# Kernel optimization log

Hardware: AMD Instinct MI355X
Metric: run time of the kernel (lower is better)

## Reference

```python
import jax, jax.numpy as jnp
import numpy as np

B, T, K, C, H = 64, 20, 5, 3, 224  # batch, candidate frames, selected frames, channels, full res
LOWD = T * 3 * 64 * 64             # 245760 flattened low-res clip


def setup_inputs() -> dict:
    key = jax.random.key(0)
    ks = jax.random.split(key, 6)
    return {
        "Full_Frame64": jax.random.normal(ks[0], (B, T, 3, 64, 64), jnp.float32),
        "Full_Frame224": jax.random.normal(ks[1], (B, T, C, H, H), jnp.float32),
        "W_skim": jax.random.normal(ks[2], (LOWD, 64), jnp.float32) * 0.01,
        "b_skim": jnp.zeros((64,), jnp.float32),
        "W_pol": jax.random.normal(ks[3], (64, 20), jnp.float32) * 0.1,
        "b_pol": jnp.zeros((20,), jnp.float32),
        "W_eval": jax.random.normal(ks[4], (K * C, 400), jnp.float32) * 0.1,
        "b_eval": jnp.zeros((400,), jnp.float32),
    }


def reference(Full_Frame64, Full_Frame224, W_skim, b_skim, W_pol, b_pol, W_eval, b_eval):
    # skim_net stub: flatten low-res clip -> 64-d feature
    fea = Full_Frame64.reshape(B, -1) @ W_skim + b_skim                 # [B,64]
    # PolicyNet (per source bug, the inner Linear(64,64) is discarded): relu -> Linear(64,20)
    logits = jax.nn.relu(fea) @ W_pol + b_pol                           # [B,20]
    dist = jax.lax.stop_gradient(jax.nn.softmax(logits, axis=1))        # detached, as in source
    # Test mode: top-5 probabilities, indices sorted ascending
    idx = jnp.sort(jax.lax.top_k(dist, K)[1], axis=1)                   # [B,5] int32
    # gather selected frames: [B,5,3,224,224]
    selected = jnp.take_along_axis(Full_Frame224, idx[:, :, None, None, None], axis=1)
    # eval_net stub: spatial mean pool -> flatten -> Linear(15,400)
    pooled = selected.mean(axis=(3, 4)).reshape(B, K * C)               # [B,15]
    out = pooled @ W_eval + b_eval                                       # [B,400]
    return out
```

## Files before the change

kernel.cpp:

```cpp
#include <hip/hip_runtime.h>
#include <float.h>

#define B_SZ   64
#define T_FR   20
#define K_SEL  5
#define C_CH   3
#define D_SKIM 245760
#define HW224  50176
#define F4_IMG 12544
#define K1_BLOCKS 768
#define K1_TILES  10
#define BK        32
#define GP_PARTS  4
#define F4_PART   3136

#define AC(v, dp) ((dp) == 0 ? (v).x : (dp) == 1 ? (v).y : (dp) == 2 ? (v).z : (v).w)

__global__ __launch_bounds__(256) void skim_gemm(
    const float* __restrict__ A, const float* __restrict__ W,
    float* __restrict__ partial) {
  __shared__ float lds[8192];
  const int t    = threadIdx.x;
  const int lane = t & 63;
  const int wav  = t >> 6;
  const int kb   = lane >> 3;
  const int b0   = kb << 3;
  const int j0   = (lane & 7) << 3;

  const int ga0 = 2 * wav;
  const int arow0 = 8 * ga0 + (lane >> 3);
  const int aslot0 = (lane & 7) ^ (ga0 & 7);
  const int arow1 = 8 * (ga0 + 1) + (lane >> 3);
  const int aslot1 = (lane & 7) ^ ((ga0 + 1) & 7);
  const int wrow0 = 4 * ga0 + (lane >> 4);
  const int wcol0 = (lane & 15) << 2;
  const int wrow1 = 4 * (ga0 + 1) + (lane >> 4);

  float acc[8][8];
#pragma unroll
  for (int i = 0; i < 8; ++i)
#pragma unroll
    for (int j = 0; j < 8; ++j) acc[i][j] = 0.f;

  const long dbase = (long)blockIdx.x * (K1_TILES * BK);

#define STAGE(bufsel, tile_)                                                   \
  {                                                                            \
    const long d0_ = dbase + (long)(tile_) * BK;                               \
    float* Ab = lds + (bufsel) * 4096;                                         \
    float* Wb = Ab + 2048;                                                     \
    __builtin_amdgcn_global_load_lds(                                          \
        (const __attribute__((address_space(1))) void*)(A + (long)arow0 * D_SKIM + d0_ + aslot0 * 4), \
        (__attribute__((address_space(3))) void*)(Ab + ga0 * 256), 16, 0, 0);  \
    __builtin_amdgcn_global_load_lds(                                          \
        (const __attribute__((address_space(1))) void*)(A + (long)arow1 * D_SKIM + d0_ + aslot1 * 4), \
        (__attribute__((address_space(3))) void*)(Ab + (ga0 + 1) * 256), 16, 0, 0); \
    __builtin_amdgcn_global_load_lds(                                          \
        (const __attribute__((address_space(1))) void*)(W + (d0_ + wrow0) * 64 + wcol0), \
        (__attribute__((address_space(3))) void*)(Wb + ga0 * 256), 16, 0, 0);  \
    __builtin_amdgcn_global_load_lds(                                          \
        (const __attribute__((address_space(1))) void*)(W + (d0_ + wrow1) * 64 + wcol0), \
        (__attribute__((address_space(3))) void*)(Wb + (ga0 + 1) * 256), 16, 0, 0); \
  }

  STAGE(0, 0)
  asm volatile("s_waitcnt vmcnt(0)" ::: "memory");
  __syncthreads();

  for (int tile = 0; tile < K1_TILES; ++tile) {
    if (tile + 1 < K1_TILES) STAGE((tile + 1) & 1, tile + 1)
    const float* Ab = lds + (tile & 1) * 4096;
    const float* Wb = Ab + 2048;
#pragma unroll
    for (int chunk = 0; chunk < 2; ++chunk) {
      const int dc = (wav << 3) + (chunk << 2);
      const int sw = dc ^ (kb << 2);
      const float4 a0 = *reinterpret_cast<const float4*>(&Ab[(b0 + 0) * 32 + sw]);
      const float4 a1 = *reinterpret_cast<const float4*>(&Ab[(b0 + 1) * 32 + sw]);
      const float4 a2 = *reinterpret_cast<const float4*>(&Ab[(b0 + 2) * 32 + sw]);
      const float4 a3 = *reinterpret_cast<const float4*>(&Ab[(b0 + 3) * 32 + sw]);
      const float4 a4 = *reinterpret_cast<const float4*>(&Ab[(b0 + 4) * 32 + sw]);
      const float4 a5 = *reinterpret_cast<const float4*>(&Ab[(b0 + 5) * 32 + sw]);
      const float4 a6 = *reinterpret_cast<const float4*>(&Ab[(b0 + 6) * 32 + sw]);
      const float4 a7 = *reinterpret_cast<const float4*>(&Ab[(b0 + 7) * 32 + sw]);
#pragma unroll
      for (int dp = 0; dp < 4; ++dp) {
        const float4 wlo = *reinterpret_cast<const float4*>(&Wb[(dc + dp) * 64 + j0]);
        const float4 whi = *reinterpret_cast<const float4*>(&Wb[(dc + dp) * 64 + j0 + 4]);
#define FMA_ROW(i, av)                             \
        acc[i][0] = fmaf(av, wlo.x, acc[i][0]);    \
        acc[i][1] = fmaf(av, wlo.y, acc[i][1]);    \
        acc[i][2] = fmaf(av, wlo.z, acc[i][2]);    \
        acc[i][3] = fmaf(av, wlo.w, acc[i][3]);    \
        acc[i][4] = fmaf(av, whi.x, acc[i][4]);    \
        acc[i][5] = fmaf(av, whi.y, acc[i][5]);    \
        acc[i][6] = fmaf(av, whi.z, acc[i][6]);    \
        acc[i][7] = fmaf(av, whi.w, acc[i][7]);
        FMA_ROW(0, AC(a0, dp)) FMA_ROW(1, AC(a1, dp))
        FMA_ROW(2, AC(a2, dp)) FMA_ROW(3, AC(a3, dp))
        FMA_ROW(4, AC(a4, dp)) FMA_ROW(5, AC(a5, dp))
        FMA_ROW(6, AC(a6, dp)) FMA_ROW(7, AC(a7, dp))
#undef FMA_ROW
      }
    }
    asm volatile("s_waitcnt vmcnt(0)" ::: "memory");
    __syncthreads();
  }
#undef STAGE

  float* reg = lds + ((wav & 1) ? 4096 : 0);
  if (wav < 2) {
#pragma unroll
    for (int i = 0; i < 8; ++i) {
      *reinterpret_cast<float4*>(&reg[(b0 + i) * 64 + j0])     =
          make_float4(acc[i][0], acc[i][1], acc[i][2], acc[i][3]);
      *reinterpret_cast<float4*>(&reg[(b0 + i) * 64 + j0 + 4]) =
          make_float4(acc[i][4], acc[i][5], acc[i][6], acc[i][7]);
    }
  }
  __syncthreads();
  if (wav >= 2) {
#pragma unroll
    for (int i = 0; i < 8; ++i) {
      float4 lo = *reinterpret_cast<const float4*>(&reg[(b0 + i) * 64 + j0]);
      float4 hi = *reinterpret_cast<const float4*>(&reg[(b0 + i) * 64 + j0 + 4]);
      lo.x += acc[i][0]; lo.y += acc[i][1]; lo.z += acc[i][2]; lo.w += acc[i][3];
      hi.x += acc[i][4]; hi.y += acc[i][5]; hi.z += acc[i][6]; hi.w += acc[i][7];
      *reinterpret_cast<float4*>(&reg[(b0 + i) * 64 + j0])     = lo;
      *reinterpret_cast<float4*>(&reg[(b0 + i) * 64 + j0 + 4]) = hi;
    }
  }
  __syncthreads();
  const float4* r0 = reinterpret_cast<const float4*>(lds);
  const float4* r1 = reinterpret_cast<const float4*>(lds + 4096);
  float4* out = reinterpret_cast<float4*>(partial + (long)blockIdx.x * 4096);
#pragma unroll
  for (int k = 0; k < 4; ++k) {
    const int e = t + k * 256;
    float4 v0 = r0[e], v1 = r1[e];
    out[e] = make_float4(v0.x + v1.x, v0.y + v1.y, v0.z + v1.z, v0.w + v1.w);
  }
}

__global__ __launch_bounds__(256) void policy_topk(
    const float* __restrict__ partial, const float* __restrict__ b_skim,
    const float* __restrict__ W_pol, const float* __restrict__ b_pol,
    int* __restrict__ idx_out) {
  const int b    = blockIdx.x;
  const int t    = threadIdx.x;
  const int lane = t & 63;
  const int wav  = t >> 6;
  __shared__ float red[4][64];
  __shared__ float vsh[64];
  __shared__ float lgsh[20];

  const int P4 = K1_BLOCKS / 4;
  const float* base = partial + (long)(wav * P4) * 4096 + b * 64 + lane;
  float s = 0.f;
#pragma unroll 16
  for (int p = 0; p < P4; ++p) s += base[(long)p * 4096];
  red[wav][lane] = s;
  __syncthreads();

  if (wav == 0) {
    float fea = ((red[0][lane] + red[1][lane]) + (red[2][lane] + red[3][lane]))
                + b_skim[lane];
    vsh[lane] = fmaxf(fea, 0.f);
  }
  __syncthreads();

  if (t < 20) {
    float lg = b_pol[t];
#pragma unroll 8
    for (int k = 0; k < 64; ++k) lg = fmaf(vsh[k], W_pol[k * 20 + t], lg);
    lgsh[t] = lg;
  }
  __syncthreads();

  if (t == 0) {
    float lg[20];
#pragma unroll
    for (int i = 0; i < 20; ++i) lg[i] = lgsh[i];
    int sel[K_SEL];
#pragma unroll
    for (int s5 = 0; s5 < K_SEL; ++s5) {
      int bi = 0; float bv = lg[0];
      for (int i = 1; i < 20; ++i)
        if (lg[i] > bv) { bv = lg[i]; bi = i; }
      sel[s5] = bi; lg[bi] = -FLT_MAX;
    }
#pragma unroll
    for (int a = 1; a < K_SEL; ++a) {
      int v = sel[a], c = a;
      while (c > 0 && sel[c - 1] > v) { sel[c] = sel[c - 1]; --c; }
      sel[c] = v;
    }
#pragma unroll
    for (int s5 = 0; s5 < K_SEL; ++s5) idx_out[b * K_SEL + s5] = sel[s5];
  }
}

__global__ __launch_bounds__(256) void gather_pool(
    const float* __restrict__ F224, const int* __restrict__ idx,
    float* __restrict__ pooled_part) {
  const int blk  = blockIdx.x;
  const int part = blk & 3;
  const int img  = blk >> 2;
  const int b = img / 15;
  const int r = img % 15;
  const int s = r / 3;
  const int c = r % 3;
  const int fr = idx[b * K_SEL + s];
  const float4* p4 = reinterpret_cast<const float4*>(F224) +
      ((long)(b * T_FR + fr) * C_CH + c) * F4_IMG + part * F4_PART;
  float sum = 0.f;
#pragma unroll 4
  for (int i = threadIdx.x; i < F4_PART; i += 256) {
    float4 v = p4[i];
    sum += (v.x + v.y) + (v.z + v.w);
  }
#pragma unroll
  for (int off = 32; off; off >>= 1) sum += __shfl_down(sum, off);
  __shared__ float red[4];
  if ((threadIdx.x & 63) == 0) red[threadIdx.x >> 6] = sum;
  __syncthreads();
  if (threadIdx.x == 0) pooled_part[blk] = (red[0] + red[1]) + (red[2] + red[3]);
}

__global__ __launch_bounds__(512) void eval_gemm(
    const float* __restrict__ pooled_part, const float* __restrict__ W_eval,
    const float* __restrict__ b_eval, float* __restrict__ out) {
  const int b = blockIdx.x;
  const int t = threadIdx.x;
  __shared__ float sh[60];
  __shared__ float pk[15];
  if (t < 60) sh[t] = pooled_part[b * 60 + t];
  __syncthreads();
  if (t < 15)
    pk[t] = ((sh[t * 4] + sh[t * 4 + 1]) + (sh[t * 4 + 2] + sh[t * 4 + 3]))
            * (1.0f / HW224);
  __syncthreads();
  if (t < 400) {
    float o = b_eval[t];
#pragma unroll
    for (int k = 0; k < 15; ++k) o = fmaf(pk[k], W_eval[k * 400 + t], o);
    out[b * 400 + t] = o;
  }
}

extern "C" void kernel_launch(void* const* d_in, const int* in_sizes, int n_in,
                              void* d_out, int out_size, void* d_ws, size_t ws_size,
                              hipStream_t stream) {
  const float* F64    = (const float*)d_in[0];
  const float* F224   = (const float*)d_in[1];
  const float* W_skim = (const float*)d_in[2];
  const float* b_skim = (const float*)d_in[3];
  const float* W_pol  = (const float*)d_in[4];
  const float* b_pol  = (const float*)d_in[5];
  const float* W_eval = (const float*)d_in[6];
  const float* b_eval = (const float*)d_in[7];
  float* out = (float*)d_out;

  char* ws = (char*)d_ws;
  float* partial     = (float*)ws;
  int*   idx         = (int*)(ws + (size_t)K1_BLOCKS * 4096 * 4);
  float* pooled_part = (float*)(ws + (size_t)K1_BLOCKS * 4096 * 4 + 1280);

  skim_gemm  <<<K1_BLOCKS, 256, 0, stream>>>(F64, W_skim, partial);
  policy_topk<<<B_SZ, 256, 0, stream>>>(partial, b_skim, W_pol, b_pol, idx);
  gather_pool<<<B_SZ * K_SEL * C_CH * GP_PARTS, 256, 0, stream>>>(F224, idx, pooled_part);
  eval_gemm  <<<B_SZ, 512, 0, stream>>>(pooled_part, W_eval, b_eval, out);
}
```

Measured before the change: 85.11 us.

## Fuse policy and eval stages via atomic arrival counters, triple-buffer skim GEMM

```diff
diff --git a/kernel.cpp b/kernel.cpp
--- a/kernel.cpp
+++ b/kernel.cpp
@@ -16,10 +16,13 @@
 
 #define AC(v, dp) ((dp) == 0 ? (v).x : (dp) == 1 ? (v).y : (dp) == 2 ? (v).z : (v).w)
 
-__global__ __launch_bounds__(256) void skim_gemm(
+__global__ __launch_bounds__(256) void skim_policy(
     const float* __restrict__ A, const float* __restrict__ W,
-    float* __restrict__ partial) {
-  __shared__ float lds[8192];
+    float* __restrict__ partial, const float* __restrict__ b_skim,
+    const float* __restrict__ W_pol, const float* __restrict__ b_pol,
+    int* __restrict__ idx_out, int* __restrict__ cnt) {
+  __shared__ float lds[12288];
+  __shared__ int s_arr;
   const int t    = threadIdx.x;
   const int lane = t & 63;
   const int wav  = t >> 6;
@@ -27,14 +30,14 @@
   const int b0   = kb << 3;
   const int j0   = (lane & 7) << 3;
 
-  const int ga0 = 2 * wav;
-  const int arow0 = 8 * ga0 + (lane >> 3);
+  const int ga0    = 2 * wav;
+  const int arow0  = 8 * ga0 + (lane >> 3);
   const int aslot0 = (lane & 7) ^ (ga0 & 7);
-  const int arow1 = 8 * (ga0 + 1) + (lane >> 3);
+  const int arow1  = 8 * (ga0 + 1) + (lane >> 3);
   const int aslot1 = (lane & 7) ^ ((ga0 + 1) & 7);
-  const int wrow0 = 4 * ga0 + (lane >> 4);
-  const int wcol0 = (lane & 15) << 2;
-  const int wrow1 = 4 * (ga0 + 1) + (lane >> 4);
+  const int wrow0  = 4 * ga0 + (lane >> 4);
+  const int wcol0  = (lane & 15) << 2;
+  const int wrow1  = 4 * (ga0 + 1) + (lane >> 4);
 
   float acc[8][8];
 #pragma unroll
@@ -64,12 +67,18 @@
   }
 
   STAGE(0, 0)
-  asm volatile("s_waitcnt vmcnt(0)" ::: "memory");
-  __syncthreads();
+  STAGE(1, 1)
 
   for (int tile = 0; tile < K1_TILES; ++tile) {
-    if (tile + 1 < K1_TILES) STAGE((tile + 1) & 1, tile + 1)
-    const float* Ab = lds + (tile & 1) * 4096;
+    if (tile < K1_TILES - 1) {
+      asm volatile("s_waitcnt vmcnt(4)" ::: "memory");
+    } else {
+      asm volatile("s_waitcnt vmcnt(0)" ::: "memory");
+    }
+    __builtin_amdgcn_sched_barrier(0);
+    __builtin_amdgcn_s_barrier();
+    if (tile + 2 < K1_TILES) STAGE((tile + 2) % 3, tile + 2)
+    const float* Ab = lds + (tile % 3) * 4096;
     const float* Wb = Ab + 2048;
 #pragma unroll
     for (int chunk = 0; chunk < 2; ++chunk) {
@@ -103,11 +112,10 @@
 #undef FMA_ROW
       }
     }
-    asm volatile("s_waitcnt vmcnt(0)" ::: "memory");
-    __syncthreads();
   }
 #undef STAGE
 
+  __syncthreads();
   float* reg = lds + ((wav & 1) ? 4096 : 0);
   if (wav < 2) {
 #pragma unroll
@@ -131,39 +139,44 @@
     }
   }
   __syncthreads();
-  const float4* r0 = reinterpret_cast<const float4*>(lds);
-  const float4* r1 = reinterpret_cast<const float4*>(lds + 4096);
-  float4* out = reinterpret_cast<float4*>(partial + (long)blockIdx.x * 4096);
-#pragma unroll
-  for (int k = 0; k < 4; ++k) {
-    const int e = t + k * 256;
-    float4 v0 = r0[e], v1 = r1[e];
-    out[e] = make_float4(v0.x + v1.x, v0.y + v1.y, v0.z + v1.z, v0.w + v1.w);
-  }
-}
-
-__global__ __launch_bounds__(256) void policy_topk(
-    const float* __restrict__ partial, const float* __restrict__ b_skim,
-    const float* __restrict__ W_pol, const float* __restrict__ b_pol,
-    int* __restrict__ idx_out) {
-  const int b    = blockIdx.x;
-  const int t    = threadIdx.x;
-  const int lane = t & 63;
-  const int wav  = t >> 6;
-  __shared__ float red[4][64];
-  __shared__ float vsh[64];
-  __shared__ float lgsh[20];
-
+  {
+    const float4* r0 = reinterpret_cast<const float4*>(lds);
+    const float4* r1 = reinterpret_cast<const float4*>(lds + 4096);
+    float4* outp = reinterpret_cast<float4*>(partial + (long)blockIdx.x * 4096);
+#pragma unroll
+    for (int k = 0; k < 4; ++k) {
+      const int e = t + k * 256;
+      float4 v0 = r0[e], v1 = r1[e];
+      outp[e] = make_float4(v0.x + v1.x, v0.y + v1.y, v0.z + v1.z, v0.w + v1.w);
+    }
+  }
+
+  __syncthreads();
+  if (t == 0)
+    s_arr = __hip_atomic_fetch_add(cnt, 1, __ATOMIC_ACQ_REL, __HIP_MEMORY_SCOPE_AGENT);
+  __syncthreads();
+  const int arr = s_arr;
+  if (arr < K1_BLOCKS - B_SZ) return;
+  const int b = arr - (K1_BLOCKS - B_SZ);
+
+  if (t == 0) {
+    while (__hip_atomic_load(cnt, __ATOMIC_ACQUIRE, __HIP_MEMORY_SCOPE_AGENT) < K1_BLOCKS) {}
+  }
+  __syncthreads();
+
+  float* red  = lds;
+  float* vsh  = lds + 256;
+  float* lgsh = lds + 320;
   const int P4 = K1_BLOCKS / 4;
   const float* base = partial + (long)(wav * P4) * 4096 + b * 64 + lane;
-  float s = 0.f;
+  float ssum = 0.f;
 #pragma unroll 16
-  for (int p = 0; p < P4; ++p) s += base[(long)p * 4096];
-  red[wav][lane] = s;
+  for (int p = 0; p < P4; ++p) ssum += base[(long)p * 4096];
+  red[wav * 64 + lane] = ssum;
   __syncthreads();
 
   if (wav == 0) {
-    float fea = ((red[0][lane] + red[1][lane]) + (red[2][lane] + red[3][lane]))
+    float fea = ((red[lane] + red[64 + lane]) + (red[128 + lane] + red[192 + lane]))
                 + b_skim[lane];
     vsh[lane] = fmaxf(fea, 0.f);
   }
@@ -200,9 +213,11 @@
   }
 }
 
-__global__ __launch_bounds__(256) void gather_pool(
+__global__ __launch_bounds__(256) void gather_eval(
     const float* __restrict__ F224, const int* __restrict__ idx,
-    float* __restrict__ pooled_part) {
+    float* __restrict__ pooled_part, const float* __restrict__ W_eval,
+    const float* __restrict__ b_eval, float* __restrict__ out,
+    int* __restrict__ cnt2) {
   const int blk  = blockIdx.x;
   const int part = blk & 3;
   const int img  = blk >> 2;
@@ -222,15 +237,16 @@
 #pragma unroll
   for (int off = 32; off; off >>= 1) sum += __shfl_down(sum, off);
   __shared__ float red[4];
+  __shared__ int s_arr;
   if ((threadIdx.x & 63) == 0) red[threadIdx.x >> 6] = sum;
   __syncthreads();
-  if (threadIdx.x == 0) pooled_part[blk] = (red[0] + red[1]) + (red[2] + red[3]);
-}
-
-__global__ __launch_bounds__(512) void eval_gemm(
-    const float* __restrict__ pooled_part, const float* __restrict__ W_eval,
-    const float* __restrict__ b_eval, float* __restrict__ out) {
-  const int b = blockIdx.x;
+  if (threadIdx.x == 0) {
+    pooled_part[blk] = (red[0] + red[1]) + (red[2] + red[3]);
+    s_arr = __hip_atomic_fetch_add(&cnt2[b], 1, __ATOMIC_ACQ_REL, __HIP_MEMORY_SCOPE_AGENT);
+  }
+  __syncthreads();
+  if (s_arr != GP_PARTS * K_SEL * C_CH - 1) return;
+
   const int t = threadIdx.x;
   __shared__ float sh[60];
   __shared__ float pk[15];
@@ -240,11 +256,11 @@
     pk[t] = ((sh[t * 4] + sh[t * 4 + 1]) + (sh[t * 4 + 2] + sh[t * 4 + 3]))
             * (1.0f / HW224);
   __syncthreads();
-  if (t < 400) {
-    float o = b_eval[t];
-#pragma unroll
-    for (int k = 0; k < 15; ++k) o = fmaf(pk[k], W_eval[k * 400 + t], o);
-    out[b * 400 + t] = o;
+  for (int n = t; n < 400; n += 256) {
+    float o = b_eval[n];
+#pragma unroll
+    for (int k = 0; k < 15; ++k) o = fmaf(pk[k], W_eval[k * 400 + n], o);
+    out[b * 400 + n] = o;
   }
 }
 
@@ -262,12 +278,15 @@
   float* out = (float*)d_out;
 
   char* ws = (char*)d_ws;
-  float* partial     = (float*)ws;
-  int*   idx         = (int*)(ws + (size_t)K1_BLOCKS * 4096 * 4);
-  float* pooled_part = (float*)(ws + (size_t)K1_BLOCKS * 4096 * 4 + 1280);
-
-  skim_gemm  <<<K1_BLOCKS, 256, 0, stream>>>(F64, W_skim, partial);
-  policy_topk<<<B_SZ, 256, 0, stream>>>(partial, b_skim, W_pol, b_pol, idx);
-  gather_pool<<<B_SZ * K_SEL * C_CH * GP_PARTS, 256, 0, stream>>>(F224, idx, pooled_part);
-  eval_gemm  <<<B_SZ, 512, 0, stream>>>(pooled_part, W_eval, b_eval, out);
+  int*   cnt1        = (int*)ws;
+  int*   cnt2        = (int*)(ws + 64);
+  int*   idx         = (int*)(ws + 512);
+  float* pooled_part = (float*)(ws + 2048);
+  float* partial     = (float*)(ws + 65536);
+
+  hipMemsetAsync(ws, 0, 512, stream);
+  skim_policy<<<K1_BLOCKS, 256, 0, stream>>>(F64, W_skim, partial, b_skim,
+                                             W_pol, b_pol, idx, cnt1);
+  gather_eval<<<B_SZ * K_SEL * C_CH * GP_PARTS, 256, 0, stream>>>(
+      F224, idx, pooled_part, W_eval, b_eval, out, cnt2);
 }
```

Result: slower. 301.1 us (+253.8%).
